# Optimization experiments

Measured on AMD Instinct MI355X. Metric: run time of the kernel, lower is better.

Reference implementation:

```python
import jax, jax.numpy as jnp
import numpy as np

NUM_EXPERTS = 3
INPUT_DIM = 1024
HIDDEN_DIM = 4096
OUTPUT_DIM = 1024
ROUTER_HIDDEN = 128
BATCH = 8192


def setup_inputs() -> dict:
    key = jax.random.key(0)
    ks = jax.random.split(key, 6)
    s_in = 1.0 / np.sqrt(INPUT_DIM)
    s_h = 1.0 / np.sqrt(HIDDEN_DIM)
    s_rh = 1.0 / np.sqrt(ROUTER_HIDDEN)
    return {
        "x": jax.random.normal(ks[0], (BATCH, INPUT_DIM), jnp.float32),
        "router_w1": jax.random.normal(ks[1], (INPUT_DIM, ROUTER_HIDDEN), jnp.float32) * s_in,
        "router_b1": jnp.zeros((ROUTER_HIDDEN,), jnp.float32),
        "router_w2": jax.random.normal(ks[2], (ROUTER_HIDDEN, NUM_EXPERTS), jnp.float32) * s_rh,
        "router_b2": jnp.zeros((NUM_EXPERTS,), jnp.float32),
        "expert_w1": jax.random.normal(ks[3], (NUM_EXPERTS, INPUT_DIM, HIDDEN_DIM), jnp.float32) * s_in,
        "expert_b1": jnp.zeros((NUM_EXPERTS, HIDDEN_DIM), jnp.float32),
        "expert_w2": jax.random.normal(ks[4], (NUM_EXPERTS, HIDDEN_DIM, OUTPUT_DIM), jnp.float32) * s_h,
        "expert_b2": jnp.zeros((NUM_EXPERTS, OUTPUT_DIM), jnp.float32),
    }


def reference(x, router_w1, router_b1, router_w2, router_b2,
              expert_w1, expert_b1, expert_w2, expert_b2):
    # Router: MLP -> softmax probs, hard top-1 selection (argmax)
    rh = jax.nn.relu(x @ router_w1 + router_b1)          # [B, 128]
    logits = rh @ router_w2 + router_b2                   # [B, E]
    probs = jax.nn.softmax(logits, axis=-1)
    selected = jnp.argmax(probs, axis=-1)                 # [B] int

    # Per-expert forward on all tokens (dense equivalent of masked dispatch)
    h = jax.nn.relu(jnp.einsum('bi,eih->ebh', x, expert_w1) + expert_b1[:, None, :])  # [E,B,H]
    y = jnp.einsum('ebh,eho->ebo', h, expert_w2) + expert_b2[:, None, :]              # [E,B,O]

    # Scatter-combine: each token takes its selected expert's output
    outputs = jnp.take_along_axis(
        y, selected[None, :, None], axis=0)[0]            # [B, O]

    # routing_stats: tokens per expert
    routing_stats = jnp.bincount(selected, length=NUM_EXPERTS)
    return outputs, routing_stats
```

## Files before the change

kernel.cpp:

```cpp
#include <hip/hip_runtime.h>
#include <hip/hip_bf16.h>

typedef short bf16x8 __attribute__((ext_vector_type(8)));
typedef float f32x4 __attribute__((ext_vector_type(4)));
typedef __attribute__((address_space(1))) const void gconst_t;
typedef __attribute__((address_space(3))) void lds_t;

#define DEVI __device__ __forceinline__

constexpr int BATCH   = 8192;
constexpr int IN_DIM  = 1024;
constexpr int HID     = 4096;
constexpr int OUT_DIM = 1024;
constexpr int NE      = 3;

constexpr size_t XBF_OFF  = 0;
constexpr size_t W1T_OFF  = 16777216;
constexpr size_t W2T_OFF  = W1T_OFF + 25165824;
constexpr size_t H_OFF    = W2T_OFF + 25165824;
constexpr size_t XLO_OFF  = H_OFF;
constexpr size_t META_OFF = H_OFF + 67108864;
constexpr size_t W3_OFF   = META_OFF + 131072;

DEVI unsigned short f2bf(float f) {
  __hip_bfloat16 h = __float2bfloat16(f);
  return *reinterpret_cast<unsigned short*>(&h);
}
DEVI float bf2f(unsigned short u) {
  unsigned v = (unsigned)u << 16;
  return __uint_as_float(v);
}

__global__ __launch_bounds__(256) void prepA_kernel(
    const float* __restrict__ x, const float* __restrict__ rw1,
    unsigned short* __restrict__ xb, unsigned short* __restrict__ xlo,
    unsigned short* __restrict__ w3) {
  __shared__ float tile[64][65];
  const int b = blockIdx.x;
  const int tid = threadIdx.x;
  if (b < 512) {
    const float4* xv4 = (const float4*)x;
    const int total = BATCH * IN_DIM / 4;
    for (int i = b * 256 + tid; i < total; i += 512 * 256) {
      const float4 v = xv4[i];
      ushort4 h, l;
      h.x = f2bf(v.x); l.x = f2bf(v.x - bf2f(h.x));
      h.y = f2bf(v.y); l.y = f2bf(v.y - bf2f(h.y));
      h.z = f2bf(v.z); l.z = f2bf(v.z - bf2f(h.z));
      h.w = f2bf(v.w); l.w = f2bf(v.w - bf2f(h.w));
      ((ushort4*)xb)[i] = h;
      ((ushort4*)xlo)[i] = l;
    }
  } else {
    const int w = b - 512;
    const int r0 = (w >> 1) * 64;
    const int c0 = (w & 1) * 64;
    const int tr = tid >> 4;
    const int tc = (tid & 15) << 2;
#pragma unroll
    for (int i = 0; i < 4; i++) {
      const int r = tr + i * 16;
      const float4 v = *(const float4*)(rw1 + (size_t)(r0 + r) * 128 + (c0 + tc));
      tile[r][tc + 0] = v.x; tile[r][tc + 1] = v.y; tile[r][tc + 2] = v.z; tile[r][tc + 3] = v.w;
    }
    __syncthreads();
#pragma unroll
    for (int i = 0; i < 4; i++) {
      const int c = tr + i * 16;
      ushort4 hi, lo;
      {
        float f;
        f = tile[tc + 0][c]; hi.x = f2bf(f); lo.x = f2bf(f - bf2f(hi.x));
        f = tile[tc + 1][c]; hi.y = f2bf(f); lo.y = f2bf(f - bf2f(hi.y));
        f = tile[tc + 2][c]; hi.z = f2bf(f); lo.z = f2bf(f - bf2f(hi.z));
        f = tile[tc + 3][c]; hi.w = f2bf(f); lo.w = f2bf(f - bf2f(hi.w));
      }
      unsigned short* base = w3 + (size_t)(c0 + c) * 3072 + (r0 + tc);
      *(ushort4*)(base)        = hi;
      *(ushort4*)(base + 1024) = hi;
      *(ushort4*)(base + 2048) = lo;
    }
  }
}

__global__ __launch_bounds__(256) void router_gemm(
    const unsigned short* __restrict__ xhi, const unsigned short* __restrict__ xlo,
    const unsigned short* __restrict__ w3, const float* __restrict__ rb1,
    const float* __restrict__ rw2, const float* __restrict__ rb2,
    int* __restrict__ counts, int* __restrict__ toklist) {
  __shared__ __align__(16) char smem[70656];
  unsigned short* Ab = (unsigned short*)smem;
  unsigned short* Bb = (unsigned short*)(smem + 24576);
  float* rhp  = (float*)smem;
  float* lgp  = (float*)(smem + 67584);
  float* rw2l = (float*)(smem + 69120);

  const int tid = threadIdx.x;
  const int m0 = blockIdx.x * 128;
  constexpr int NT = 96;

  int tokA[2], kelA[2];
  unsigned aoff[2];
  const unsigned short* bsrc[2];
  unsigned boff[2];
#pragma unroll
  for (int l = 0; l < 2; l++) {
    const unsigned o = l * 4096u + (unsigned)tid * 16u;
    const unsigned p = o ^ (((o >> 6) & 3u) << 4);
    const int row = (int)(o >> 6);
    const int kel = (int)((p & 63u) >> 1);
    aoff[l] = o;
    tokA[l] = m0 + row;
    kelA[l] = kel;
    boff[l] = o;
    bsrc[l] = w3 + (size_t)row * 3072 + kel;
  }

  auto STAGE = [&](int buf, int t) {
    const int seg = t >> 5;
    const int kin = (t & 31) * 32;
    const unsigned short* abase = (seg == 1) ? xlo : xhi;
#pragma unroll
    for (int l = 0; l < 2; l++)
      __builtin_amdgcn_global_load_lds(
          (gconst_t*)(abase + (size_t)tokA[l] * 1024 + kin + kelA[l]),
          (lds_t*)((char*)Ab + buf * 8192 + aoff[l]), 16, 0, 0);
#pragma unroll
    for (int l = 0; l < 2; l++)
      __builtin_amdgcn_global_load_lds(
          (gconst_t*)(bsrc[l] + t * 32),
          (lds_t*)((char*)Bb + buf * 8192 + boff[l]), 16, 0, 0);
  };

  f32x4 acc[4][4];
#pragma unroll
  for (int i = 0; i < 4; i++)
#pragma unroll
    for (int j = 0; j < 4; j++) acc[i][j] = {0.f, 0.f, 0.f, 0.f};

  const int lane = tid & 63;
  const int wave = tid >> 6;
  const int wm = (wave >> 1) * 64;
  const int wn = (wave & 1) * 64;
  const int fr = lane & 15;
  const int fc = lane >> 4;

  STAGE(0, 0);
  STAGE(1, 1);

  int cur = 0;
  for (int t = 0; t < NT; ++t) {
    if (t + 1 < NT) asm volatile("s_waitcnt vmcnt(4)" ::: "memory");
    else            asm volatile("s_waitcnt vmcnt(0)" ::: "memory");
    __builtin_amdgcn_sched_barrier(0);
    __builtin_amdgcn_s_barrier();
    __builtin_amdgcn_sched_barrier(0);
    bf16x8 af[4], bv[4];
#pragma unroll
    for (int m = 0; m < 4; m++) {
      const unsigned row = (unsigned)(wm + m * 16 + fr);
      const unsigned addr = ((row << 6) + (unsigned)(fc << 4)) ^ ((row & 3u) << 4);
      af[m] = *(const bf16x8*)((const char*)Ab + cur * 8192 + addr);
    }
#pragma unroll
    for (int n = 0; n < 4; n++) {
      const unsigned row = (unsigned)(wn + n * 16 + fr);
      const unsigned addr = ((row << 6) + (unsigned)(fc << 4)) ^ ((row & 3u) << 4);
      bv[n] = *(const bf16x8*)((const char*)Bb + cur * 8192 + addr);
    }
    asm volatile("s_waitcnt lgkmcnt(0)" ::: "memory");
    __builtin_amdgcn_sched_barrier(0);
    __builtin_amdgcn_s_setprio(1);
#pragma unroll
    for (int m = 0; m < 4; m++)
#pragma unroll
      for (int n = 0; n < 4; n++)
        acc[m][n] = __builtin_amdgcn_mfma_f32_16x16x32_bf16(af[m], bv[n], acc[m][n], 0, 0, 0);
    __builtin_amdgcn_s_setprio(0);
    if (t + 2 < NT) {
      const int nb = (cur + 2 >= 3) ? cur - 1 : cur + 2;
      STAGE(nb, t + 2);
    }
    cur = (cur + 1 == 3) ? 0 : cur + 1;
  }

  __syncthreads();

  for (int i = tid; i < 384; i += 256) rw2l[i] = rw2[i];

  const int crow = (lane >> 4) * 4;
  const int ccol = lane & 15;
  float b1v[4];
#pragma unroll
  for (int ni = 0; ni < 4; ni++) b1v[ni] = rb1[wn + ni * 16 + ccol];
#pragma unroll
  for (int mi = 0; mi < 4; mi++) {
#pragma unroll
    for (int r = 0; r < 4; r++) {
      const int tokL = wm + mi * 16 + crow + r;
#pragma unroll
      for (int ni = 0; ni < 4; ni++) {
        const int h = wn + ni * 16 + ccol;
        rhp[tokL * 132 + h] = fmaxf(acc[mi][ni][r] + b1v[ni], 0.f);
      }
    }
  }
  __syncthreads();

#pragma unroll
  for (int pass = 0; pass < 2; ++pass) {
    const int t = tid + pass * 256;
    if (t < 384) {
      const int tok = t / 3, e = t - tok * 3;
      float s = rb2[e];
#pragma unroll 4
      for (int j = 0; j < 128; ++j) s = fmaf(rhp[tok * 132 + j], rw2l[j * 3 + e], s);
      lgp[tok * 3 + e] = s;
    }
  }
  __syncthreads();

  if (tid < 128) {
    const float l0 = lgp[tid * 3], l1 = lgp[tid * 3 + 1], l2 = lgp[tid * 3 + 2];
    int sel = 0; float m = l0;
    if (l1 > m) { m = l1; sel = 1; }
    if (l2 > m) { m = l2; sel = 2; }
    const int slot = atomicAdd(&counts[sel], 1);
    toklist[sel * BATCH + slot] = m0 + tid;
  }
}

__global__ __launch_bounds__(256) void prep2_kernel(
    const float* __restrict__ ew1, const float* __restrict__ ew2,
    unsigned short* __restrict__ w1t, unsigned short* __restrict__ w2t) {
  __shared__ float tile[64][65];
  const int b = blockIdx.x;
  const int tid = threadIdx.x;

  const float* src; unsigned short* dst; int R, C, r0, c0;
  if (b < 3072) {
    const int e = b / 1024, w = b % 1024;
    src = ew1 + (size_t)e * 1024 * 4096; dst = w1t + (size_t)e * 4096 * 1024;
    R = 1024; C = 4096; r0 = (w & 15) * 64; c0 = (w >> 4) * 64;
  } else {
    const int bb = b - 3072, e = bb / 1024, w = bb % 1024;
    src = ew2 + (size_t)e * 4096 * 1024; dst = w2t + (size_t)e * 1024 * 4096;
    R = 4096; C = 1024; r0 = (w & 63) * 64; c0 = (w >> 6) * 64;
  }
  const int tr = tid >> 4;
  const int tc = (tid & 15) << 2;
#pragma unroll
  for (int i = 0; i < 4; i++) {
    const int r = tr + i * 16;
    const float4 v = *(const float4*)(src + (size_t)(r0 + r) * C + (c0 + tc));
    tile[r][tc + 0] = v.x; tile[r][tc + 1] = v.y; tile[r][tc + 2] = v.z; tile[r][tc + 3] = v.w;
  }
  __syncthreads();
#pragma unroll
  for (int i = 0; i < 4; i++) {
    const int c = tr + i * 16;
    ushort4 o;
    o.x = f2bf(tile[tc + 0][c]);
    o.y = f2bf(tile[tc + 1][c]);
    o.z = f2bf(tile[tc + 2][c]);
    o.w = f2bf(tile[tc + 3][c]);
    *(ushort4*)(dst + (size_t)(c0 + c) * R + (r0 + tc)) = o;
  }
}

template <int MODE>
__global__ __launch_bounds__(512, 2) void moe_gemm(
    const unsigned short* __restrict__ Abase, const unsigned short* __restrict__ Ball,
    const float* __restrict__ biasAll, unsigned short* __restrict__ Hout,
    float* __restrict__ Yout, const int* __restrict__ toklist, const int* __restrict__ counts,
    float* __restrict__ tail) {
  constexpr int N  = (MODE == 0) ? HID : OUT_DIM;
  constexpr int K  = (MODE == 0) ? IN_DIM : HID;
  constexpr int NT = K / 32;

  const int tid = threadIdx.x;
  if (MODE == 0 && blockIdx.x == 0 && blockIdx.y == 0 && tid < NE)
    tail[tid] = (float)counts[tid];

  const int c0 = counts[0], c1 = counts[1], c2 = counts[2];
  const int mb0 = (c0 + 127) >> 7, mb1 = (c1 + 127) >> 7, mb2 = (c2 + 127) >> 7;
  const int bx = blockIdx.x;
  int e, mblk;
  if (bx < mb0) { e = 0; mblk = bx; }
  else if (bx < mb0 + mb1) { e = 1; mblk = bx - mb0; }
  else if (bx < mb0 + mb1 + mb2) { e = 2; mblk = bx - mb0 - mb1; }
  else return;
  const int cnt = (e == 0) ? c0 : (e == 1) ? c1 : c2;
  const int m0 = mblk * 128;
  const int n0 = blockIdx.y * 256;
  const int off_e = (e > 0 ? c0 : 0) + (e > 1 ? c1 : 0);
  const unsigned short* Bmat = Ball + (size_t)e * ((size_t)N * K);
  const float* bias = biasAll + (size_t)e * N;

  __shared__ unsigned short Ab[3][128 * 32];
  __shared__ unsigned short Bb[3][256 * 32];

  const unsigned short* asrc;
  const unsigned short* bsrc[2];
  unsigned aoff, boff[2];
  {
    const unsigned o = (unsigned)tid * 16u;
    const unsigned p = o ^ (((o >> 6) & 3u) << 4);
    const int row = (int)(o >> 6);
    const int kel = (int)((p & 63u) >> 1);
    aoff = o;
    int slot = m0 + row; if (slot > cnt - 1) slot = cnt - 1;
    const size_t arow = (MODE == 0) ? (size_t)toklist[e * BATCH + slot]
                                    : (size_t)(off_e + slot);
    asrc = Abase + arow * K + kel;
  }
#pragma unroll
  for (int l = 0; l < 2; l++) {
    const unsigned o = l * 8192u + (unsigned)tid * 16u;
    const unsigned p = o ^ (((o >> 6) & 3u) << 4);
    const int row = (int)(o >> 6);
    const int kel = (int)((p & 63u) >> 1);
    boff[l] = o;
    bsrc[l] = Bmat + (size_t)(n0 + row) * K + kel;
  }

  f32x4 acc[4][4];
#pragma unroll
  for (int i = 0; i < 4; i++)
#pragma unroll
    for (int j = 0; j < 4; j++) acc[i][j] = {0.f, 0.f, 0.f, 0.f};

  const int lane = tid & 63;
  const int wave = tid >> 6;
  const int wm = (wave >> 2) * 64;
  const int wn = (wave & 3) * 64;
  const int fr = lane & 15;
  const int fc = lane >> 4;

  auto STAGE = [&](int buf, int kofs) {
    __builtin_amdgcn_global_load_lds((gconst_t*)(asrc + kofs),
                                     (lds_t*)((char*)&Ab[buf][0] + aoff), 16, 0, 0);
#pragma unroll
    for (int l = 0; l < 2; l++)
      __builtin_amdgcn_global_load_lds((gconst_t*)(bsrc[l] + kofs),
                                       (lds_t*)((char*)&Bb[buf][0] + boff[l]), 16, 0, 0);
  };

  STAGE(0, 0);
  STAGE(1, 32);

  int cur = 0;
  for (int t = 0; t < NT; ++t) {
    if (t + 1 < NT) asm volatile("s_waitcnt vmcnt(3)" ::: "memory");
    else            asm volatile("s_waitcnt vmcnt(0)" ::: "memory");
    __builtin_amdgcn_sched_barrier(0);
    __builtin_amdgcn_s_barrier();
    __builtin_amdgcn_sched_barrier(0);
    bf16x8 af[4], bv[4];
#pragma unroll
    for (int m = 0; m < 4; m++) {
      const unsigned row = (unsigned)(wm + m * 16 + fr);
      const unsigned addr = ((row << 6) + (unsigned)(fc << 4)) ^ ((row & 3u) << 4);
      af[m] = *(const bf16x8*)((const char*)&Ab[cur][0] + addr);
    }
#pragma unroll
    for (int n = 0; n < 4; n++) {
      const unsigned row = (unsigned)(wn + n * 16 + fr);
      const unsigned addr = ((row << 6) + (unsigned)(fc << 4)) ^ ((row & 3u) << 4);
      bv[n] = *(const bf16x8*)((const char*)&Bb[cur][0] + addr);
    }
    asm volatile("s_waitcnt lgkmcnt(0)" ::: "memory");
    __builtin_amdgcn_sched_barrier(0);
    __builtin_amdgcn_s_setprio(1);
#pragma unroll
    for (int m = 0; m < 4; m++)
#pragma unroll
      for (int n = 0; n < 4; n++)
        acc[m][n] = __builtin_amdgcn_mfma_f32_16x16x32_bf16(af[m], bv[n], acc[m][n], 0, 0, 0);
    __builtin_amdgcn_s_setprio(0);
    if (t + 2 < NT) {
      const int nb = (cur + 2 >= 3) ? cur - 1 : cur + 2;
      STAGE(nb, (t + 2) * 32);
    }
    cur = (cur + 1 == 3) ? 0 : cur + 1;
  }

  const int crow = (lane >> 4) * 4;
  const int ccol = lane & 15;
#pragma unroll
  for (int mi = 0; mi < 4; mi++) {
#pragma unroll
    for (int r = 0; r < 4; r++) {
      const int slot = m0 + wm + mi * 16 + crow + r;
      if (slot >= cnt) continue;
      if (MODE == 0) {
        unsigned short* hrow = Hout + (size_t)(off_e + slot) * HID;
#pragma unroll
        for (int ni = 0; ni < 4; ni++) {
          const int n = n0 + wn + ni * 16 + ccol;
          const float v = acc[mi][ni][r] + bias[n];
          hrow[n] = f2bf(fmaxf(v, 0.f));
        }
      } else {
        const int tok = toklist[e * BATCH + slot];
        float* yrow = Yout + (size_t)tok * OUT_DIM;
#pragma unroll
        for (int ni = 0; ni < 4; ni++) {
          const int n = n0 + wn + ni * 16 + ccol;
          yrow[n] = acc[mi][ni][r] + bias[n];
        }
      }
    }
  }
}

extern "C" void kernel_launch(void* const* d_in, const int* in_sizes, int n_in,
                              void* d_out, int out_size, void* d_ws, size_t ws_size,
                              hipStream_t stream) {
  const float* x   = (const float*)d_in[0];
  const float* rw1 = (const float*)d_in[1];
  const float* rb1 = (const float*)d_in[2];
  const float* rw2 = (const float*)d_in[3];
  const float* rb2 = (const float*)d_in[4];
  const float* ew1 = (const float*)d_in[5];
  const float* eb1 = (const float*)d_in[6];
  const float* ew2 = (const float*)d_in[7];
  const float* eb2 = (const float*)d_in[8];
  float* out = (float*)d_out;

  char* ws = (char*)d_ws;
  unsigned short* xb  = (unsigned short*)(ws + XBF_OFF);
  unsigned short* w1t = (unsigned short*)(ws + W1T_OFF);
  unsigned short* w2t = (unsigned short*)(ws + W2T_OFF);
  unsigned short* h   = (unsigned short*)(ws + H_OFF);
  unsigned short* xlo = (unsigned short*)(ws + XLO_OFF);
  int* counts  = (int*)(ws + META_OFF);
  int* toklist = counts + 16;
  unsigned short* w3 = (unsigned short*)(ws + W3_OFF);
  float* tail = out + (size_t)BATCH * OUT_DIM;

  hipMemsetAsync(counts, 0, 64, stream);
  prepA_kernel<<<544, 256, 0, stream>>>(x, rw1, xb, xlo, w3);
  router_gemm<<<64, 256, 0, stream>>>(xb, xlo, w3, rb1, rw2, rb2, counts, toklist);
  prep2_kernel<<<6144, 256, 0, stream>>>(ew1, ew2, w1t, w2t);
  moe_gemm<0><<<dim3(66, 16), 512, 0, stream>>>(xb, w1t, eb1, h, nullptr, toklist, counts, tail);
  moe_gemm<1><<<dim3(66, 4), 512, 0, stream>>>(h, w2t, eb2, nullptr, out, toklist, counts, tail);
}
```

Baseline: 367.7 us.

## Issue next-stage prefetch before LDS reads and widen LDS XOR swizzle

Moves the global->LDS prefetch for stage t+2 to right after the barrier, so the loads are issued before the MFMA block instead of after it, and drops the explicit lgkmcnt wait plus sched barrier so the compiler can interleave LDS reads with MFMAs. Replaces the 2-bit row XOR swizzle with a 3-bit swizzle keyed on bits 7-9 to reduce LDS bank conflicts on the 16-byte fragment reads. Loading now uses an inverse mapping (row taken from the swizzled address). With a 3-buffer ring, issuing the prefetch earlier relies on the barrier to keep the buffer being refilled apart from the one still being read.

```diff
diff --git a/kernel.cpp b/kernel.cpp
--- a/kernel.cpp
+++ b/kernel.cpp
@@ -30,6 +30,8 @@
   unsigned v = (unsigned)u << 16;
   return __uint_as_float(v);
 }
+
+DEVI unsigned swz(unsigned b) { return b ^ (((b >> 7) & 7u) << 4); }
 
 __global__ __launch_bounds__(256) void prepA_kernel(
     const float* __restrict__ x, const float* __restrict__ rw1,
@@ -106,8 +108,8 @@
 #pragma unroll
   for (int l = 0; l < 2; l++) {
     const unsigned o = l * 4096u + (unsigned)tid * 16u;
-    const unsigned p = o ^ (((o >> 6) & 3u) << 4);
-    const int row = (int)(o >> 6);
+    const unsigned p = swz(o);
+    const int row = (int)(p >> 6);
     const int kel = (int)((p & 63u) >> 1);
     aoff[l] = o;
     tokA[l] = m0 + row;
@@ -155,21 +157,21 @@
     __builtin_amdgcn_sched_barrier(0);
     __builtin_amdgcn_s_barrier();
     __builtin_amdgcn_sched_barrier(0);
+    if (t + 2 < NT) {
+      const int nb = (cur + 2 >= 3) ? cur - 1 : cur + 2;
+      STAGE(nb, t + 2);
+    }
     bf16x8 af[4], bv[4];
 #pragma unroll
     for (int m = 0; m < 4; m++) {
-      const unsigned row = (unsigned)(wm + m * 16 + fr);
-      const unsigned addr = ((row << 6) + (unsigned)(fc << 4)) ^ ((row & 3u) << 4);
-      af[m] = *(const bf16x8*)((const char*)Ab + cur * 8192 + addr);
+      const unsigned L = (unsigned)(wm + m * 16 + fr) * 64u + (unsigned)(fc << 4);
+      af[m] = *(const bf16x8*)((const char*)Ab + cur * 8192 + swz(L));
     }
 #pragma unroll
     for (int n = 0; n < 4; n++) {
-      const unsigned row = (unsigned)(wn + n * 16 + fr);
-      const unsigned addr = ((row << 6) + (unsigned)(fc << 4)) ^ ((row & 3u) << 4);
-      bv[n] = *(const bf16x8*)((const char*)Bb + cur * 8192 + addr);
-    }
-    asm volatile("s_waitcnt lgkmcnt(0)" ::: "memory");
-    __builtin_amdgcn_sched_barrier(0);
+      const unsigned L = (unsigned)(wn + n * 16 + fr) * 64u + (unsigned)(fc << 4);
+      bv[n] = *(const bf16x8*)((const char*)Bb + cur * 8192 + swz(L));
+    }
     __builtin_amdgcn_s_setprio(1);
 #pragma unroll
     for (int m = 0; m < 4; m++)
@@ -177,10 +179,6 @@
       for (int n = 0; n < 4; n++)
         acc[m][n] = __builtin_amdgcn_mfma_f32_16x16x32_bf16(af[m], bv[n], acc[m][n], 0, 0, 0);
     __builtin_amdgcn_s_setprio(0);
-    if (t + 2 < NT) {
-      const int nb = (cur + 2 >= 3) ? cur - 1 : cur + 2;
-      STAGE(nb, t + 2);
-    }
     cur = (cur + 1 == 3) ? 0 : cur + 1;
   }
 
@@ -305,8 +303,8 @@
   unsigned aoff, boff[2];
   {
     const unsigned o = (unsigned)tid * 16u;
-    const unsigned p = o ^ (((o >> 6) & 3u) << 4);
-    const int row = (int)(o >> 6);
+    const unsigned p = swz(o);
+    const int row = (int)(p >> 6);
     const int kel = (int)((p & 63u) >> 1);
     aoff = o;
     int slot = m0 + row; if (slot > cnt - 1) slot = cnt - 1;
@@ -317,8 +315,8 @@
 #pragma unroll
   for (int l = 0; l < 2; l++) {
     const unsigned o = l * 8192u + (unsigned)tid * 16u;
-    const unsigned p = o ^ (((o >> 6) & 3u) << 4);
-    const int row = (int)(o >> 6);
+    const unsigned p = swz(o);
+    const int row = (int)(p >> 6);
     const int kel = (int)((p & 63u) >> 1);
     boff[l] = o;
     bsrc[l] = Bmat + (size_t)(n0 + row) * K + kel;
@@ -356,21 +354,21 @@
     __builtin_amdgcn_sched_barrier(0);
     __builtin_amdgcn_s_barrier();
     __builtin_amdgcn_sched_barrier(0);
+    if (t + 2 < NT) {
+      const int nb = (cur + 2 >= 3) ? cur - 1 : cur + 2;
+      STAGE(nb, (t + 2) * 32);
+    }
     bf16x8 af[4], bv[4];
 #pragma unroll
     for (int m = 0; m < 4; m++) {
-      const unsigned row = (unsigned)(wm + m * 16 + fr);
-      const unsigned addr = ((row << 6) + (unsigned)(fc << 4)) ^ ((row & 3u) << 4);
-      af[m] = *(const bf16x8*)((const char*)&Ab[cur][0] + addr);
+      const unsigned L = (unsigned)(wm + m * 16 + fr) * 64u + (unsigned)(fc << 4);
+      af[m] = *(const bf16x8*)((const char*)&Ab[cur][0] + swz(L));
     }
 #pragma unroll
     for (int n = 0; n < 4; n++) {
-      const unsigned row = (unsigned)(wn + n * 16 + fr);
-      const unsigned addr = ((row << 6) + (unsigned)(fc << 4)) ^ ((row & 3u) << 4);
-      bv[n] = *(const bf16x8*)((const char*)&Bb[cur][0] + addr);
-    }
-    asm volatile("s_waitcnt lgkmcnt(0)" ::: "memory");
-    __builtin_amdgcn_sched_barrier(0);
+      const unsigned L = (unsigned)(wn + n * 16 + fr) * 64u + (unsigned)(fc << 4);
+      bv[n] = *(const bf16x8*)((const char*)&Bb[cur][0] + swz(L));
+    }
     __builtin_amdgcn_s_setprio(1);
 #pragma unroll
     for (int m = 0; m < 4; m++)
@@ -378,10 +376,6 @@
       for (int n = 0; n < 4; n++)
         acc[m][n] = __builtin_amdgcn_mfma_f32_16x16x32_bf16(af[m], bv[n], acc[m][n], 0, 0, 0);
     __builtin_amdgcn_s_setprio(0);
-    if (t + 2 < NT) {
-      const int nb = (cur + 2 >= 3) ? cur - 1 : cur + 2;
-      STAGE(nb, (t + 2) * 32);
-    }
     cur = (cur + 1 == 3) ? 0 : cur + 1;
   }
 
```

After: 376.2 us. +2.3%, slower.
